# Performance work log

Hardware: AMD Instinct MI355X
Metric: run time of the kernel (lower is better)

The kernel has to match this reference:

```python
import jax, jax.numpy as jnp
import numpy as np

EMBED_DIM = 1024
HEAD_DIM = 64


def setup_inputs() -> dict:
    key = jax.random.key(0)
    ks = jax.random.split(key, 7)
    B, S = 4, 2048
    x = jax.random.normal(ks[0], (B, S, EMBED_DIM), dtype=jnp.float32)
    s = EMBED_DIM ** -0.5  # torch Linear default init scale (uniform bound)
    Wk = jax.random.uniform(ks[1], (EMBED_DIM, HEAD_DIM), minval=-s, maxval=s)
    bk = jax.random.uniform(ks[2], (HEAD_DIM,), minval=-s, maxval=s)
    Wq = jax.random.uniform(ks[3], (EMBED_DIM, HEAD_DIM), minval=-s, maxval=s)
    bq = jax.random.uniform(ks[4], (HEAD_DIM,), minval=-s, maxval=s)
    Wv = jax.random.uniform(ks[5], (EMBED_DIM, HEAD_DIM), minval=-s, maxval=s)
    bv = jax.random.uniform(ks[6], (HEAD_DIM,), minval=-s, maxval=s)
    return {"x": x, "Wq": Wq, "bq": bq, "Wk": Wk, "bk": bk, "Wv": Wv, "bv": bv}


def reference(x, Wq, bq, Wk, bk, Wv, bv):
    # projections: [B,S,D]
    q = x @ Wq + bq
    k = x @ Wk + bk
    v = x @ Wv + bv
    # NOTE: faithful to source, which DIVIDES by head_dim**-0.5 (i.e. multiplies by sqrt(d))
    scale = HEAD_DIM ** -0.5
    wei = jnp.einsum('bqd,bkd->bqk', q, k) / scale  # [B,S,S]
    S = x.shape[1]
    causal = jnp.tril(jnp.ones((S, S), dtype=bool))
    wei = jnp.where(causal, wei, -jnp.inf)
    attn_weights = jax.nn.softmax(wei, axis=-1)
    return jnp.einsum('bqk,bkd->bqd', attn_weights, v)
```

## Files before the change

kernel.cpp:

```cpp
#include <hip/hip_runtime.h>
#include <math.h>

#define S_LEN 2048
#define NB 4
#define EMB 1024
#define HD 64
#define NROW (NB * S_LEN)
#define NEG_BIG -3.0e38f
#define SC 11.5415603f
#define DEFER_THR 3.0f
#define KVSPLIT 4

typedef _Float16 half8 __attribute__((ext_vector_type(8)));
typedef _Float16 half4 __attribute__((ext_vector_type(4)));
typedef float f32x4 __attribute__((ext_vector_type(4)));

static __device__ __forceinline__ f32x4 mfma32(half8 a, half8 b, f32x4 c) {
    return __builtin_amdgcn_mfma_f32_16x16x32_f16(a, b, c, 0, 0, 0);
}
static __device__ __forceinline__ f32x4 mfma16(half4 a, half4 b, f32x4 c) {
    return __builtin_amdgcn_mfma_f32_16x16x16f16(a, b, c, 0, 0, 0);
}

__global__ __launch_bounds__(256) void prep_w(
    const float* __restrict__ Wq, const float* __restrict__ Wk,
    const float* __restrict__ Wv, _Float16* __restrict__ wt_frag)
{
    const int g  = blockIdx.x >> 4;
    const int kc = blockIdx.x & 15;
    const int k0 = kc * 64;
    const float* W = (g == 0) ? Wq : (g == 1) ? Wk : Wv;

    __shared__ float tile[64][68];
    const int t = threadIdx.x;
    {
        const int kk = t >> 2, cb = (t & 3) * 16;
#pragma unroll
        for (int i = 0; i < 4; i++)
            *(f32x4*)&tile[kk][cb + 4 * i] =
                *(const f32x4*)(W + (size_t)(k0 + kk) * HD + cb + 4 * i);
    }
    __syncthreads();

    const int c4 = t >> 6, l = t & 63;
    const int col = c4 * 16 + (l & 15);
    const int krow = (l >> 4) * 8;
#pragma unroll
    for (int sub = 0; sub < 2; sub++) {
        half8 hv;
#pragma unroll
        for (int e = 0; e < 8; e++)
            hv[e] = (_Float16)tile[sub * 32 + krow + e][col];
        const size_t addr = (size_t)(g * 4 + c4) * 16384 +
                            (size_t)(kc * 2 + sub) * 512 + (size_t)l * 8;
        *(half8*)(wt_frag + addr) = hv;
    }
}

__global__ __launch_bounds__(768) void proj_kernel(
    const float* __restrict__ x, const _Float16* __restrict__ wt_frag,
    const float* __restrict__ bq, const float* __restrict__ bk,
    const float* __restrict__ bv,
    _Float16* __restrict__ qs, _Float16* __restrict__ kh_,
    _Float16* __restrict__ vt)
{
    const int m0 = blockIdx.x * 32;
    const int t = threadIdx.x, lane = t & 63, w = t >> 6;

    __shared__ __align__(16) _Float16 xs[32][1032];

    for (int i = t; i < 4096; i += 768) {
        const int row = i >> 7, off = (i & 127) * 8;
        const float* xp = x + (size_t)(m0 + row) * EMB + off;
        const f32x4 v0 = *(const f32x4*)xp;
        const f32x4 v1 = *(const f32x4*)(xp + 4);
        half8 h;
#pragma unroll
        for (int jj = 0; jj < 4; jj++) {
            h[jj]     = (_Float16)v0[jj];
            h[4 + jj] = (_Float16)v1[jj];
        }
        *(half8*)&xs[row][off] = h;
    }

    const int f = w;
    const int row0 = lane & 15, kq = lane >> 4;
    const _Float16* wp = wt_frag + (size_t)f * 16384 + (size_t)lane * 8;

    half8 wbuf[4];
#pragma unroll
    for (int c = 0; c < 4; c++) wbuf[c] = *(const half8*)(wp + (size_t)c * 512);

    __syncthreads();

    f32x4 acc0 = f32x4{0, 0, 0, 0}, acc1 = f32x4{0, 0, 0, 0};

#pragma unroll
    for (int c = 0; c < 32; ++c) {
        const half8 ax0 = *(const half8*)&xs[row0][c * 32 + kq * 8];
        const half8 ax1 = *(const half8*)&xs[16 + row0][c * 32 + kq * 8];
        const half8 bw = wbuf[c & 3];
        acc0 = mfma32(ax0, bw, acc0);
        acc1 = mfma32(ax1, bw, acc1);
        if (c + 4 < 32) wbuf[c & 3] = *(const half8*)(wp + (size_t)(c + 4) * 512);
    }

    const int mat = f >> 2, c4 = f & 3;
    const int mcol = c4 * 16 + (lane & 15);
    const float bb = ((mat == 0) ? bq : (mat == 1) ? bk : bv)[mcol];
#pragma unroll
    for (int rh = 0; rh < 2; rh++) {
        const f32x4 acc = rh ? acc1 : acc0;
        const int grow0 = m0 + rh * 16 + kq * 4;
        if (mat == 0) {
#pragma unroll
            for (int r = 0; r < 4; r++)
                qs[(size_t)(grow0 + r) * HD + mcol] = (_Float16)((acc[r] + bb) * SC);
        } else if (mat == 1) {
#pragma unroll
            for (int r = 0; r < 4; r++)
                kh_[(size_t)(grow0 + r) * HD + mcol] = (_Float16)(acc[r] + bb);
        } else {
            half4 hv;
#pragma unroll
            for (int r = 0; r < 4; r++) hv[r] = (_Float16)(acc[r] + bb);
            const int bidx = grow0 >> 11, sr = grow0 & (S_LEN - 1);
            *(half4*)(vt + ((size_t)bidx * HD + mcol) * S_LEN + sr) = hv;
        }
    }
}

__global__ __launch_bounds__(512, 6) void attn_kernel(
    const _Float16* __restrict__ qs, const _Float16* __restrict__ kh_,
    const _Float16* __restrict__ vt,
    _Float16* __restrict__ po, float* __restrict__ pm, float* __restrict__ pl)
{
    const int id = blockIdx.x;
    const int qq = id & 3;
    const int b  = (id >> 2) & 3;
    const int qt = 31 - (id >> 4);
    const int q0 = qt * 64;
    const int t = threadIdx.x, lane = t & 63, w = t >> 6;
    const int rf = w >> 1, kvh = w & 1;

    __shared__ __align__(16) unsigned char smem[37888];
    _Float16 (*klds)[64][72] = (_Float16(*)[64][72])smem;
    _Float16 (*vlds)[64][72] = (_Float16(*)[64][72])(smem + 18432);
    float (*obuf)[16][68] = (float(*)[16][68])smem;
    float* mbuf = (float*)(smem + 36864);
    float* lbuf = (float*)(smem + 36864 + 512);

    const size_t rowq = ((size_t)b * S_LEN + q0 + rf * 16 + (lane & 15)) * HD + (lane >> 4) * 8;
    const half8 bq0 = *(const half8*)(qs + rowq);
    const half8 bq1 = *(const half8*)(qs + rowq + 32);

    f32x4 o[4];
#pragma unroll
    for (int c = 0; c < 4; c++) o[c] = f32x4{0, 0, 0, 0};
    float m_r = NEG_BIG, l_r = 0.f;

    const int nt = qt + 1;
    const int lo = (nt * qq) >> 2, hi = (nt * (qq + 1)) >> 2;

    const size_t kbase = (size_t)b * S_LEN * HD;
    const size_t vbase = (size_t)b * HD * S_LEN;
    const int srow = t >> 3, scol = (t & 7) * 8;

    half8 sK, sV;
    auto gload = [&](int tl) {
        sK = *(const half8*)(kh_ + kbase + (size_t)(tl * 64 + srow) * HD + scol);
        sV = *(const half8*)(vt + vbase + (size_t)srow * S_LEN + tl * 64 + scol);
    };
    auto swrite = [&](int nb) {
        *(half8*)&klds[nb][srow][scol] = sK;
        *(half8*)&vlds[nb][srow][scol] = sV;
    };

    if (lo < hi) { gload(lo); swrite(0); }
    __syncthreads();

    const int qrow_min = q0 + rf * 16;

    int cur = 0;
    for (int tl = lo; tl < hi; ++tl) {
        if (tl + 1 < hi) gload(tl + 1);

        const int kv0 = tl * 64 + kvh * 32;
        __builtin_amdgcn_s_setprio(1);
        f32x4 s[2];
#pragma unroll
        for (int h = 0; h < 2; h++) {
            const int keyl = kvh * 32 + 16 * h + (lane & 15);
            f32x4 a = f32x4{0, 0, 0, 0};
            a = mfma32(*(const half8*)&klds[cur][keyl][(lane >> 4) * 8], bq0, a);
            a = mfma32(*(const half8*)&klds[cur][keyl][32 + (lane >> 4) * 8], bq1, a);
            s[h] = a;
        }
        __builtin_amdgcn_s_setprio(0);

        float tv[8];
        if (kv0 + 31 <= qrow_min) {
#pragma unroll
            for (int h = 0; h < 2; h++)
#pragma unroll
                for (int r = 0; r < 4; r++) tv[h * 4 + r] = s[h][r];
        } else {
            const int qrow = q0 + rf * 16 + (lane & 15);
            const int kb0  = kv0 + (lane >> 4) * 4;
#pragma unroll
            for (int h = 0; h < 2; h++)
#pragma unroll
                for (int r = 0; r < 4; r++)
                    tv[h * 4 + r] = (kb0 + 16 * h + r <= qrow) ? s[h][r] : NEG_BIG;
        }

        float mt = tv[0];
#pragma unroll
        for (int i = 1; i < 8; i++) mt = fmaxf(mt, tv[i]);
        mt = fmaxf(mt, __shfl_xor(mt, 16));
        mt = fmaxf(mt, __shfl_xor(mt, 32));

        if (!__all(mt <= m_r + DEFER_THR)) {
            const float mn = fmaxf(m_r, mt);
            const float corr = exp2f(m_r - mn);
            m_r = mn;
            l_r *= corr;
            float corrB[4];
#pragma unroll
            for (int r = 0; r < 4; r++) corrB[r] = __shfl(corr, (lane >> 4) * 4 + r);
#pragma unroll
            for (int c = 0; c < 4; c++)
#pragma unroll
                for (int r = 0; r < 4; r++) o[c][r] *= corrB[r];
        }

        float p[8], rs = 0.f;
#pragma unroll
        for (int i = 0; i < 8; i++) { p[i] = exp2f(tv[i] - m_r); rs += p[i]; }
        rs += __shfl_xor(rs, 16);
        rs += __shfl_xor(rs, 32);
        l_r += rs;

        half4 pa[2];
#pragma unroll
        for (int h = 0; h < 2; h++)
#pragma unroll
            for (int r = 0; r < 4; r++) pa[h][r] = (_Float16)p[h * 4 + r];
        __builtin_amdgcn_s_setprio(1);
#pragma unroll
        for (int c = 0; c < 4; c++) {
#pragma unroll
            for (int h = 0; h < 2; h++) {
                const half4 vf = *(const half4*)&vlds[cur][16 * c + (lane & 15)]
                                                    [kvh * 32 + 16 * h + (lane >> 4) * 4];
                o[c] = mfma16(pa[h], vf, o[c]);
            }
        }
        __builtin_amdgcn_s_setprio(0);

        if (tl + 1 < hi) swrite(cur ^ 1);
        __syncthreads();
        cur ^= 1;
    }

    if (lane < 16) { mbuf[w * 16 + lane] = m_r; lbuf[w * 16 + lane] = l_r; }
#pragma unroll
    for (int c = 0; c < 4; c++)
#pragma unroll
        for (int r = 0; r < 4; r++)
            obuf[w][(lane >> 4) * 4 + r][16 * c + (lane & 15)] = o[c][r];
    __syncthreads();

    if (t < 256) {
        const int row16 = t >> 4, cb = (t & 15) * 4;
#pragma unroll
        for (int rf2 = 0; rf2 < 4; rf2++) {
            const int w0 = rf2 * 2, w1 = w0 + 1;
            const float m0v = mbuf[w0 * 16 + row16], m1v = mbuf[w1 * 16 + row16];
            const float M = fmaxf(m0v, m1v);
            const float e0 = exp2f(m0v - M), e1 = exp2f(m1v - M);
            const float L = lbuf[w0 * 16 + row16] * e0 + lbuf[w1 * 16 + row16] * e1;
            const f32x4 o0 = *(const f32x4*)&obuf[w0][row16][cb];
            const f32x4 o1 = *(const f32x4*)&obuf[w1][row16][cb];
            half4 hv;
#pragma unroll
            for (int jj = 0; jj < 4; jj++) hv[jj] = (_Float16)(o0[jj] * e0 + o1[jj] * e1);
            const size_t idx = (size_t)(qq * NB + b) * S_LEN + q0 + rf2 * 16 + row16;
            *(half4*)(po + idx * HD + cb) = hv;
            if ((t & 15) == 0) { pm[idx] = M; pl[idx] = L; }
        }
    }
}

__global__ __launch_bounds__(256) void merge_kernel(
    const _Float16* __restrict__ po, const float* __restrict__ pm,
    const float* __restrict__ pl, float* __restrict__ out)
{
    const int b = blockIdx.y;
    const int row = blockIdx.x * 16 + (threadIdx.x >> 4);
    const int cb = (threadIdx.x & 15) * 4;

    float mv[KVSPLIT];
    float M = NEG_BIG;
#pragma unroll
    for (int qq = 0; qq < KVSPLIT; qq++) {
        mv[qq] = pm[(size_t)(qq * NB + b) * S_LEN + row];
        M = fmaxf(M, mv[qq]);
    }
    float L = 0.f;
    f32x4 acc = f32x4{0, 0, 0, 0};
#pragma unroll
    for (int qq = 0; qq < KVSPLIT; qq++) {
        const size_t idx = (size_t)(qq * NB + b) * S_LEN + row;
        const float e = exp2f(mv[qq] - M);
        L += pl[idx] * e;
        const half4 ov = *(const half4*)(po + idx * HD + cb);
#pragma unroll
        for (int jj = 0; jj < 4; jj++) acc[jj] += (float)ov[jj] * e;
    }
    const float inv = 1.0f / L;
    f32x4 res;
#pragma unroll
    for (int jj = 0; jj < 4; jj++) res[jj] = acc[jj] * inv;
    *(f32x4*)(out + ((size_t)b * S_LEN + row) * HD + cb) = res;
}

extern "C" void kernel_launch(void* const* d_in, const int* in_sizes, int n_in,
                              void* d_out, int out_size, void* d_ws, size_t ws_size,
                              hipStream_t stream) {
    const float* x  = (const float*)d_in[0];
    const float* Wq = (const float*)d_in[1];
    const float* bq = (const float*)d_in[2];
    const float* Wk = (const float*)d_in[3];
    const float* bk = (const float*)d_in[4];
    const float* Wv = (const float*)d_in[5];
    const float* bv = (const float*)d_in[6];
    float* out = (float*)d_out;

    _Float16* ws = (_Float16*)d_ws;
    const size_t nW = (size_t)192 * EMB;
    const size_t n  = (size_t)NROW * HD;
    _Float16* wt_frag = ws;
    _Float16* qsb = wt_frag + nW;
    _Float16* khb = qsb + n;
    _Float16* vtb = khb + n;
    _Float16* po = vtb + n;
    float* pm = (float*)(po + (size_t)KVSPLIT * NB * S_LEN * HD);
    float* pl = pm + (size_t)KVSPLIT * NB * S_LEN;

    prep_w<<<48, 256, 0, stream>>>(Wq, Wk, Wv, wt_frag);
    proj_kernel<<<NROW / 32, 768, 0, stream>>>(
        x, wt_frag, bq, bk, bv, qsb, khb, vtb);
    attn_kernel<<<32 * NB * KVSPLIT, 512, 0, stream>>>(qsb, khb, vtb, po, pm, pl);
    merge_kernel<<<dim3(S_LEN / 16, NB), 256, 0, stream>>>(po, pm, pl, out);
}
```

Measured before the change: 36.35 us.

## Store V in MFMA fragment layout and load directly to registers

The projection kernel now writes V in a pre-swizzled per-tile fragment layout that matches the B-operand of the 16x16x16 MFMA. The attention kernel loads those fragments straight from global memory into registers each tile, so the V staging into LDS and the LDS reads are gone. This frees LDS and cuts shared-memory traffic, but each wave now issues uncached global loads per tile that are not double-buffered like K. Their latency may be exposed, and register pressure rises under the 6-wave launch bound.

```diff
diff --git a/kernel.cpp b/kernel.cpp
--- a/kernel.cpp
+++ b/kernel.cpp
@@ -62,7 +62,7 @@
     const float* __restrict__ bq, const float* __restrict__ bk,
     const float* __restrict__ bv,
     _Float16* __restrict__ qs, _Float16* __restrict__ kh_,
-    _Float16* __restrict__ vt)
+    _Float16* __restrict__ vfrag)
 {
     const int m0 = blockIdx.x * 32;
     const int t = threadIdx.x, lane = t & 63, w = t >> 6;
@@ -125,14 +125,16 @@
 #pragma unroll
             for (int r = 0; r < 4; r++) hv[r] = (_Float16)(acc[r] + bb);
             const int bidx = grow0 >> 11, sr = grow0 & (S_LEN - 1);
-            *(half4*)(vt + ((size_t)bidx * HD + mcol) * S_LEN + sr) = hv;
+            const int T = sr >> 6, g16 = (sr >> 4) & 3;
+            *(half4*)(vfrag + ((((size_t)bidx * 32 + T) * 4 + g16) * 4 + c4) * 256
+                            + (size_t)lane * 4) = hv;
         }
     }
 }
 
 __global__ __launch_bounds__(512, 6) void attn_kernel(
     const _Float16* __restrict__ qs, const _Float16* __restrict__ kh_,
-    const _Float16* __restrict__ vt,
+    const _Float16* __restrict__ vfrag,
     _Float16* __restrict__ po, float* __restrict__ pm, float* __restrict__ pl)
 {
     const int id = blockIdx.x;
@@ -143,12 +145,11 @@
     const int t = threadIdx.x, lane = t & 63, w = t >> 6;
     const int rf = w >> 1, kvh = w & 1;
 
-    __shared__ __align__(16) unsigned char smem[37888];
+    __shared__ __align__(16) unsigned char smem[35840];
     _Float16 (*klds)[64][72] = (_Float16(*)[64][72])smem;
-    _Float16 (*vlds)[64][72] = (_Float16(*)[64][72])(smem + 18432);
     float (*obuf)[16][68] = (float(*)[16][68])smem;
-    float* mbuf = (float*)(smem + 36864);
-    float* lbuf = (float*)(smem + 36864 + 512);
+    float* mbuf = (float*)(smem + 34816);
+    float* lbuf = (float*)(smem + 34816 + 512);
 
     const size_t rowq = ((size_t)b * S_LEN + q0 + rf * 16 + (lane & 15)) * HD + (lane >> 4) * 8;
     const half8 bq0 = *(const half8*)(qs + rowq);
@@ -163,17 +164,14 @@
     const int lo = (nt * qq) >> 2, hi = (nt * (qq + 1)) >> 2;
 
     const size_t kbase = (size_t)b * S_LEN * HD;
-    const size_t vbase = (size_t)b * HD * S_LEN;
     const int srow = t >> 3, scol = (t & 7) * 8;
 
-    half8 sK, sV;
+    half8 sK;
     auto gload = [&](int tl) {
         sK = *(const half8*)(kh_ + kbase + (size_t)(tl * 64 + srow) * HD + scol);
-        sV = *(const half8*)(vt + vbase + (size_t)srow * S_LEN + tl * 64 + scol);
     };
     auto swrite = [&](int nb) {
         *(half8*)&klds[nb][srow][scol] = sK;
-        *(half8*)&vlds[nb][srow][scol] = sV;
     };
 
     if (lo < hi) { gload(lo); swrite(0); }
@@ -184,6 +182,15 @@
     int cur = 0;
     for (int tl = lo; tl < hi; ++tl) {
         if (tl + 1 < hi) gload(tl + 1);
+
+        const _Float16* vtb = vfrag + (((size_t)b * 32 + tl) * 16) * 256
+                                    + (size_t)(kvh * 2) * 4 * 256 + (size_t)lane * 4;
+        half4 vf[8];
+#pragma unroll
+        for (int c = 0; c < 4; c++)
+#pragma unroll
+            for (int h = 0; h < 2; h++)
+                vf[c * 2 + h] = *(const half4*)(vtb + (h * 4 + c) * 256);
 
         const int kv0 = tl * 64 + kvh * 32;
         __builtin_amdgcn_s_setprio(1);
@@ -249,12 +256,8 @@
         __builtin_amdgcn_s_setprio(1);
 #pragma unroll
         for (int c = 0; c < 4; c++) {
-#pragma unroll
-            for (int h = 0; h < 2; h++) {
-                const half4 vf = *(const half4*)&vlds[cur][16 * c + (lane & 15)]
-                                                    [kvh * 32 + 16 * h + (lane >> 4) * 4];
-                o[c] = mfma16(pa[h], vf, o[c]);
-            }
+            o[c] = mfma16(pa[0], vf[c * 2 + 0], o[c]);
+            o[c] = mfma16(pa[1], vf[c * 2 + 1], o[c]);
         }
         __builtin_amdgcn_s_setprio(0);
 
@@ -343,14 +346,14 @@
     _Float16* wt_frag = ws;
     _Float16* qsb = wt_frag + nW;
     _Float16* khb = qsb + n;
-    _Float16* vtb = khb + n;
-    _Float16* po = vtb + n;
+    _Float16* vfb = khb + n;
+    _Float16* po = vfb + n;
     float* pm = (float*)(po + (size_t)KVSPLIT * NB * S_LEN * HD);
     float* pl = pm + (size_t)KVSPLIT * NB * S_LEN;
 
     prep_w<<<48, 256, 0, stream>>>(Wq, Wk, Wv, wt_frag);
     proj_kernel<<<NROW / 32, 768, 0, stream>>>(
-        x, wt_frag, bq, bk, bv, qsb, khb, vtb);
-    attn_kernel<<<32 * NB * KVSPLIT, 512, 0, stream>>>(qsb, khb, vtb, po, pm, pl);
+        x, wt_frag, bq, bk, bv, qsb, khb, vfb);
+    attn_kernel<<<32 * NB * KVSPLIT, 512, 0, stream>>>(qsb, khb, vfb, po, pm, pl);
     merge_kernel<<<dim3(S_LEN / 16, NB), 256, 0, stream>>>(po, pm, pl, out);
 }
```

Result: slower. 40.87 us (+12.4%).
